# Optimization experiments

Hardware: AMD Instinct MI355X
Metric: run time of the kernel (lower is better)

## Reference

```python
import jax, jax.numpy as jnp
import numpy as np

N_EMBD = 384
N_HEAD = 6
HEAD_SIZE = N_EMBD // N_HEAD  # 64
BLOCK = 64
EPS = 1e-5


def _layernorm(x, g, b):
    mu = jnp.mean(x, axis=-1, keepdims=True)
    var = jnp.mean(jnp.square(x - mu), axis=-1, keepdims=True)
    return (x - mu) * jax.lax.rsqrt(var + EPS) * g + b


def setup_inputs() -> dict:
    key = jax.random.key(0)
    ks = jax.random.split(key, 12)
    s = 0.02
    return {
        "x": jax.random.normal(ks[0], (1024, BLOCK, N_EMBD), dtype=jnp.float32),
        "ln1_g": jnp.ones((N_EMBD,), jnp.float32),
        "ln1_b": jnp.zeros((N_EMBD,), jnp.float32),
        "Wq": jax.random.normal(ks[1], (N_HEAD, N_EMBD, HEAD_SIZE), jnp.float32) * s,
        "Wk": jax.random.normal(ks[2], (N_HEAD, N_EMBD, HEAD_SIZE), jnp.float32) * s,
        "Wv": jax.random.normal(ks[3], (N_HEAD, N_EMBD, HEAD_SIZE), jnp.float32) * s,
        "Wo": jax.random.normal(ks[4], (N_EMBD, N_EMBD), jnp.float32) * s,
        "bo": jnp.zeros((N_EMBD,), jnp.float32),
        "ln2_g": jnp.ones((N_EMBD,), jnp.float32),
        "ln2_b": jnp.zeros((N_EMBD,), jnp.float32),
        "W1": jax.random.normal(ks[5], (N_EMBD, 4 * N_EMBD), jnp.float32) * s,
        "b1": jnp.zeros((4 * N_EMBD,), jnp.float32),
        "W2": jax.random.normal(ks[6], (4 * N_EMBD, N_EMBD), jnp.float32) * s,
        "b2": jnp.zeros((N_EMBD,), jnp.float32),
    }


def reference(x, ln1_g, ln1_b, Wq, Wk, Wv, Wo, bo, ln2_g, ln2_b, W1, b1, W2, b2):
    B, T, C = x.shape
    # --- multi-head causal self-attention on ln1(x) ---
    xn = _layernorm(x, ln1_g, ln1_b)
    q = jnp.einsum('btc,hcd->bhtd', xn, Wq)
    k = jnp.einsum('btc,hcd->bhtd', xn, Wk)
    v = jnp.einsum('btc,hcd->bhtd', xn, Wv)
    scale = HEAD_SIZE ** -0.5
    att = jnp.einsum('bhtd,bhsd->bhts', q, k) * scale
    causal = jnp.tril(jnp.ones((T, T), bool))
    att = jnp.where(causal, att, -jnp.inf)
    att = jax.nn.softmax(att, axis=-1)  # dropout is identity at eval
    out = jnp.einsum('bhts,bhsd->bhtd', att, v)
    out = out.transpose(0, 2, 1, 3).reshape(B, T, C)  # concat heads
    x = x + out @ Wo + bo
    # --- feed-forward on ln2(x) ---
    xn2 = _layernorm(x, ln2_g, ln2_b)
    h = jax.nn.relu(xn2 @ W1 + b1)
    x = x + h @ W2 + b2
    return x
```

## Files before the change

kernel.cpp:

```cpp
#include <hip/hip_runtime.h>

#define TT 64
#define CC 384
#define NH 6
#define HID 1536
#define LDX 392
#define LDH 72

typedef __bf16 bf16x8 __attribute__((ext_vector_type(8)));
typedef float f32x4 __attribute__((ext_vector_type(4)));
typedef unsigned short us8 __attribute__((ext_vector_type(8)));

#define MFMA(a, b, c) __builtin_amdgcn_mfma_f32_16x16x32_bf16(a, b, c, 0, 0, 0)
#define WAITVM(N) asm volatile("s_waitcnt vmcnt(" #N ")" ::: "memory")

static __device__ __forceinline__ unsigned short f2bf(float f) {
  unsigned u = __builtin_bit_cast(unsigned, f);
  u += 0x7FFFu + ((u >> 16) & 1u);
  return (unsigned short)(u >> 16);
}
static __device__ __forceinline__ float bf2f(unsigned short h) {
  unsigned u = ((unsigned)h) << 16;
  return __builtin_bit_cast(float, u);
}
static __device__ __forceinline__ bf16x8 ld8(const unsigned short* p) {
  return __builtin_bit_cast(bf16x8, *reinterpret_cast<const us8*>(p));
}
static __device__ __forceinline__ void glds16(const unsigned short* g, unsigned short* l) {
  __builtin_amdgcn_global_load_lds(
      (const __attribute__((address_space(1))) void*)g,
      (__attribute__((address_space(3))) void*)l, 16, 0, 0);
}

__global__ void prep_w(const float* __restrict__ Wq, const float* __restrict__ Wk,
                       const float* __restrict__ Wv, const float* __restrict__ Wo,
                       const float* __restrict__ W1, const float* __restrict__ W2,
                       unsigned short* __restrict__ ws) {
  const int T0 = 1152 * 384;
  const int T1 = T0 + 384 * 384;
  const int T2 = T1 + 1536 * 384;
  const int T3 = T2 + 384 * 1536;
  for (int i = blockIdx.x * blockDim.x + threadIdx.x; i < T3; i += gridDim.x * blockDim.x) {
    float v;
    if (i < T0) {
      int n = i / 384, k = i % 384;
      int hh = n / 192, j = n % 192;
      const float* W = (j < 64) ? Wq : (j < 128) ? Wk : Wv;
      int d = (j < 64) ? j : (j < 128) ? j - 64 : j - 128;
      v = W[((size_t)hh * 384 + k) * 64 + d];
    } else if (i < T1) {
      int i2 = i - T0; int n = i2 / 384, k = i2 % 384;
      v = Wo[(size_t)k * 384 + n];
    } else if (i < T2) {
      int i2 = i - T1; int n = i2 / 384, k = i2 % 384;
      v = W1[(size_t)k * 1536 + n];
    } else {
      int i2 = i - T2; int n = i2 / 1536, k = i2 % 1536;
      v = W2[(size_t)k * 384 + n];
    }
    ws[i] = f2bf(v);
  }
}

__global__ __launch_bounds__(256, 2)
void attn_fwd(const float* __restrict__ x,
              const float* __restrict__ ln1g, const float* __restrict__ ln1b,
              const float* __restrict__ bo,
              const unsigned short* __restrict__ Wqkv,
              const unsigned short* __restrict__ WoT,
              float* __restrict__ x2) {
  __shared__ unsigned short sXN[TT * LDX];
  __shared__ unsigned short sHEAD[3 * TT * LDH];
  unsigned short* sQ = sHEAD;
  unsigned short* sK = sHEAD + TT * LDH;
  unsigned short* sV = sHEAD + 2 * TT * LDH;

  const int b = blockIdx.x;
  const int tid = threadIdx.x;
  const int wv = tid >> 6;
  const int ln = tid & 63;
  const int l16 = ln & 15;
  const int lg = ln >> 4;
  const float* xb = x + (size_t)b * TT * CC;
  const f32x4 Z4 = {0.f, 0.f, 0.f, 0.f};

#pragma unroll 1
  for (int r = wv * 16; r < wv * 16 + 16; ++r) {
    float v[6], s = 0.f, sq = 0.f;
#pragma unroll
    for (int j = 0; j < 6; ++j) { v[j] = xb[r * CC + ln + 64 * j]; s += v[j]; sq += v[j] * v[j]; }
#pragma unroll
    for (int off = 32; off; off >>= 1) { s += __shfl_xor(s, off); sq += __shfl_xor(sq, off); }
    float mu = s * (1.f / CC);
    float rs = rsqrtf(sq * (1.f / CC) - mu * mu + 1e-5f);
#pragma unroll
    for (int j = 0; j < 6; ++j) {
      int c = ln + 64 * j;
      sXN[r * LDX + c] = f2bf((v[j] - mu) * rs * ln1g[c] + ln1b[c]);
    }
  }
  __syncthreads();

  f32x4 pacc[4][6];
#pragma unroll
  for (int m = 0; m < 4; ++m)
#pragma unroll
    for (int c = 0; c < 6; ++c) pacc[m][c] = Z4;

  const unsigned short* prow[6];
#pragma unroll
  for (int c = 0; c < 6; ++c)
    prow[c] = WoT + (size_t)(wv * 96 + c * 16 + l16) * CC + 8 * lg;

#pragma unroll 1
  for (int h = 0; h < NH; ++h) {
    const unsigned short* wrow[3];
#pragma unroll
    for (int c = 0; c < 3; ++c)
      wrow[c] = Wqkv + (size_t)(h * 192 + wv * 48 + c * 16 + l16) * CC + 8 * lg;

    f32x4 qacc[4][3];
#pragma unroll
    for (int m = 0; m < 4; ++m)
#pragma unroll
      for (int c = 0; c < 3; ++c) qacc[m][c] = Z4;

    bf16x8 bpre[2][3];
#pragma unroll
    for (int c = 0; c < 3; ++c) bpre[0][c] = ld8(wrow[c] + 0);
#pragma unroll
    for (int c = 0; c < 3; ++c) bpre[1][c] = ld8(wrow[c] + 32);
#pragma unroll
    for (int kk = 0; kk < CC; kk += 32) {
      const int slot = (kk >> 5) & 1;
      bf16x8 bcur[3];
#pragma unroll
      for (int c = 0; c < 3; ++c) bcur[c] = bpre[slot][c];
      if (kk + 64 < CC) {
#pragma unroll
        for (int c = 0; c < 3; ++c) bpre[slot][c] = ld8(wrow[c] + kk + 64);
      }
      bf16x8 a[4];
#pragma unroll
      for (int m = 0; m < 4; ++m)
        a[m] = ld8(&sXN[(m * 16 + l16) * LDX + kk + 8 * lg]);
      __builtin_amdgcn_s_setprio(1);
#pragma unroll
      for (int c = 0; c < 3; ++c)
#pragma unroll
        for (int m = 0; m < 4; ++m) qacc[m][c] = MFMA(a[m], bcur[c], qacc[m][c]);
      __builtin_amdgcn_s_setprio(0);
    }
    __syncthreads();
#pragma unroll
    for (int m = 0; m < 4; ++m)
#pragma unroll
      for (int c = 0; c < 3; ++c) {
        int n = wv * 48 + c * 16 + l16;
#pragma unroll
        for (int rg = 0; rg < 4; ++rg) {
          int t = m * 16 + lg * 4 + rg;
          unsigned short bv = f2bf(qacc[m][c][rg]);
          if (n < 64) sQ[t * LDH + n] = bv;
          else if (n < 128) sK[t * LDH + (n - 64)] = bv;
          else sV[(n - 128) * LDH + t] = bv;
        }
      }
    __syncthreads();

    f32x4 sacc[4];
#pragma unroll
    for (int c = 0; c < 4; ++c) sacc[c] = Z4;
#pragma unroll
    for (int kk = 0; kk < 64; kk += 32) {
      bf16x8 a = ld8(&sQ[(wv * 16 + l16) * LDH + kk + 8 * lg]);
#pragma unroll
      for (int c = 0; c < 4; ++c) {
        bf16x8 bb = ld8(&sK[(c * 16 + l16) * LDH + kk + 8 * lg]);
        sacc[c] = MFMA(a, bb, sacc[c]);
      }
    }
#pragma unroll
    for (int rg = 0; rg < 4; ++rg) {
      int row = wv * 16 + lg * 4 + rg;
      float e[4], mx = -1e30f;
#pragma unroll
      for (int c = 0; c < 4; ++c) {
        int col = c * 16 + l16;
        float vv = sacc[c][rg] * 0.125f;
        e[c] = (col <= row) ? vv : -1e30f;
        mx = fmaxf(mx, e[c]);
      }
#pragma unroll
      for (int off = 8; off; off >>= 1) mx = fmaxf(mx, __shfl_xor(mx, off));
      float sum = 0.f;
#pragma unroll
      for (int c = 0; c < 4; ++c) {
        int col = c * 16 + l16;
        e[c] = (col <= row) ? __expf(e[c] - mx) : 0.f;
        sum += e[c];
      }
#pragma unroll
      for (int off = 8; off; off >>= 1) sum += __shfl_xor(sum, off);
      float inv = 1.f / sum;
#pragma unroll
      for (int c = 0; c < 4; ++c)
        sQ[row * LDH + c * 16 + l16] = f2bf(e[c] * inv);
    }

    bf16x8 pb[2][6];
#pragma unroll
    for (int s2 = 0; s2 < 2; ++s2)
#pragma unroll
      for (int c = 0; c < 6; ++c)
        pb[s2][c] = ld8(prow[c] + h * 64 + 32 * s2);

    f32x4 oacc[4];
#pragma unroll
    for (int c = 0; c < 4; ++c) oacc[c] = Z4;
#pragma unroll
    for (int kk = 0; kk < 64; kk += 32) {
      bf16x8 a = ld8(&sQ[(wv * 16 + l16) * LDH + kk + 8 * lg]);
#pragma unroll
      for (int c = 0; c < 4; ++c) {
        bf16x8 bb = ld8(&sV[(c * 16 + l16) * LDH + kk + 8 * lg]);
        oacc[c] = MFMA(a, bb, oacc[c]);
      }
    }
    __syncthreads();
#pragma unroll
    for (int c = 0; c < 4; ++c)
#pragma unroll
      for (int rg = 0; rg < 4; ++rg) {
        int t = wv * 16 + lg * 4 + rg;
        sK[t * LDH + c * 16 + l16] = f2bf(oacc[c][rg]);
      }
    __syncthreads();

    __builtin_amdgcn_s_setprio(1);
#pragma unroll
    for (int kk = 0; kk < 64; kk += 32) {
      const int slot = kk >> 5;
      bf16x8 a[4];
#pragma unroll
      for (int m = 0; m < 4; ++m)
        a[m] = ld8(&sK[(m * 16 + l16) * LDH + kk + 8 * lg]);
#pragma unroll
      for (int c = 0; c < 6; ++c)
#pragma unroll
        for (int m = 0; m < 4; ++m) pacc[m][c] = MFMA(a[m], pb[slot][c], pacc[m][c]);
    }
    __builtin_amdgcn_s_setprio(0);
  }

  float* xo = x2 + (size_t)b * TT * CC;
#pragma unroll
  for (int m = 0; m < 4; ++m)
#pragma unroll
    for (int c = 0; c < 6; ++c) {
      int n = wv * 96 + c * 16 + l16;
      float bov = bo[n];
#pragma unroll
      for (int rg = 0; rg < 4; ++rg) {
        int t = m * 16 + lg * 4 + rg;
        xo[t * CC + n] = xb[t * CC + n] + pacc[m][c][rg] + bov;
      }
    }
}

__global__ __launch_bounds__(256, 2)
void mlp_fwd(const float* __restrict__ ln2g, const float* __restrict__ ln2b,
             const float* __restrict__ b1, const float* __restrict__ b2,
             const unsigned short* __restrict__ W1T,
             const unsigned short* __restrict__ W2T,
             float* xo) {
  __shared__ unsigned short sXN[24576];
  __shared__ unsigned short sH[8192];
  __shared__ unsigned short sW[8192];

  const int b = blockIdx.x;
  const int tid = threadIdx.x;
  const int wv = tid >> 6;
  const int ln = tid & 63;
  const int l16 = ln & 15;
  const int lg = ln >> 4;
  float* xb = xo + (size_t)b * TT * CC;
  const f32x4 Z4 = {0.f, 0.f, 0.f, 0.f};
  unsigned short* myW = sW + wv * 2048;
  const int rx = (l16 ^ lg) << 3;

#pragma unroll 1
  for (int r = wv * 16; r < wv * 16 + 16; ++r) {
    float v[6], s = 0.f, sq = 0.f;
#pragma unroll
    for (int j = 0; j < 6; ++j) { v[j] = xb[r * CC + ln + 64 * j]; s += v[j]; sq += v[j] * v[j]; }
#pragma unroll
    for (int off = 32; off; off >>= 1) { s += __shfl_xor(s, off); sq += __shfl_xor(sq, off); }
    float mu = s * (1.f / CC);
    float rs = rsqrtf(sq * (1.f / CC) - mu * mu + 1e-5f);
    int m = r >> 4, row16 = r & 15;
#pragma unroll
    for (int j = 0; j < 6; ++j) {
      int c = ln + 64 * j;
      int sl = c >> 5, ks = (c >> 3) & 3, off = c & 7;
      sXN[(((m * 12 + sl) * 4 + ks) * 16 + (row16 ^ ks)) * 8 + off] =
          f2bf((v[j] - mu) * rs * ln2g[c] + ln2b[c]);
    }
  }
  __syncthreads();

#define G1S(CH, SL) do {                                                        \
    _Pragma("unroll")                                                           \
    for (int j = 0; j < 2; ++j)                                                 \
      glds16(W1T + (size_t)((CH) * 128 + wv * 32 + j * 16 + (ln >> 2)) * CC +   \
                 (SL) * 32 + (ln & 3) * 8,                                      \
             myW + ((SL) & 1) * 1024 + j * 512);                                \
  } while (0)

#define G1C(SL) do {                                                            \
    bf16x8 a_[4];                                                               \
    _Pragma("unroll")                                                           \
    for (int m = 0; m < 4; ++m)                                                 \
      a_[m] = ld8(&sXN[((m * 48 + (SL) * 4 + lg) << 7) + rx]);                  \
    __builtin_amdgcn_s_setprio(1);                                              \
    _Pragma("unroll")                                                           \
    for (int c = 0; c < 2; ++c) {                                               \
      bf16x8 bb_ = ld8(&myW[((SL) & 1) * 1024 + c * 512 + l16 * 32 + lg * 8]);  \
      _Pragma("unroll")                                                         \
      for (int m = 0; m < 4; ++m) hacc[m][c] = MFMA(a_[m], bb_, hacc[m][c]);    \
    }                                                                           \
    __builtin_amdgcn_s_setprio(0);                                              \
  } while (0)

  f32x4 macc[4][6];
#pragma unroll
  for (int m = 0; m < 4; ++m)
#pragma unroll
    for (int c = 0; c < 6; ++c) macc[m][c] = Z4;

  const unsigned short* w2base = W2T + (size_t)(wv * 96 + l16) * HID + 8 * lg;

  G1S(0, 0);

#pragma unroll 1
  for (int ch = 0; ch < 12; ++ch) {
    f32x4 hacc[4][2];
#pragma unroll
    for (int m = 0; m < 4; ++m)
#pragma unroll
      for (int c = 0; c < 2; ++c) hacc[m][c] = Z4;

    G1S(ch, 1);  WAITVM(2); G1C(0);
    G1S(ch, 2);  WAITVM(2); G1C(1);
    G1S(ch, 3);  WAITVM(2); G1C(2);
    G1S(ch, 4);  WAITVM(2); G1C(3);
    G1S(ch, 5);  WAITVM(2); G1C(4);
    G1S(ch, 6);  WAITVM(2); G1C(5);
    G1S(ch, 7);  WAITVM(2); G1C(6);
    G1S(ch, 8);  WAITVM(2); G1C(7);
    G1S(ch, 9);  WAITVM(2); G1C(8);
    G1S(ch, 10); WAITVM(2); G1C(9);
    G1S(ch, 11); WAITVM(2); G1C(10);
    WAITVM(0);   G1C(11);

    float b1c[2];
#pragma unroll
    for (int c = 0; c < 2; ++c) b1c[c] = b1[ch * 128 + wv * 32 + c * 16 + l16];
    const unsigned short* w2p = w2base + ch * 128;
    bf16x8 c2[6];
#pragma unroll
    for (int c = 0; c < 6; ++c) c2[c] = ld8(w2p + (size_t)(c * 16) * HID);
    if (ch < 11) G1S(ch + 1, 0);

    __syncthreads();

#pragma unroll
    for (int m = 0; m < 4; ++m)
#pragma unroll
      for (int c = 0; c < 2; ++c) {
        int nl = wv * 32 + c * 16 + l16;
        int slh = nl >> 5, ks = (nl >> 3) & 3, off = nl & 7;
#pragma unroll
        for (int rg = 0; rg < 4; ++rg) {
          int row16 = lg * 4 + rg;
          sH[(((m * 4 + slh) * 4 + ks) * 16 + (row16 ^ ks)) * 8 + off] =
              f2bf(fmaxf(hacc[m][c][rg] + b1c[c], 0.f));
        }
      }
    __syncthreads();

#pragma unroll
    for (int sl = 0; sl < 4; ++sl) {
      bf16x8 a2[4];
#pragma unroll
      for (int m = 0; m < 4; ++m)
        a2[m] = ld8(&sH[((m * 16 + sl * 4 + lg) << 7) + rx]);
      bf16x8 nxt[6];
      if (sl < 3) {
#pragma unroll
        for (int c = 0; c < 6; ++c) nxt[c] = ld8(w2p + (size_t)(c * 16) * HID + (sl + 1) * 32);
      }
      __builtin_amdgcn_s_setprio(1);
#pragma unroll
      for (int c = 0; c < 6; ++c)
#pragma unroll
        for (int m = 0; m < 4; ++m) macc[m][c] = MFMA(a2[m], c2[c], macc[m][c]);
      __builtin_amdgcn_s_setprio(0);
      if (sl < 3) {
#pragma unroll
        for (int c = 0; c < 6; ++c) c2[c] = nxt[c];
      }
    }
  }

#pragma unroll
  for (int m = 0; m < 4; ++m)
#pragma unroll
    for (int c = 0; c < 6; ++c) {
      int n = wv * 96 + c * 16 + l16;
      float b2v = b2[n];
#pragma unroll
      for (int rg = 0; rg < 4; ++rg) {
        int t = m * 16 + lg * 4 + rg;
        size_t idx = (size_t)t * CC + n;
        float x2v = xb[idx];
        xb[idx] = x2v + macc[m][c][rg] + b2v;
      }
    }
#undef G1S
#undef G1C
}

extern "C" void kernel_launch(void* const* d_in, const int* in_sizes, int n_in,
                              void* d_out, int out_size, void* d_ws, size_t ws_size,
                              hipStream_t stream) {
  const float* x    = (const float*)d_in[0];
  const float* ln1g = (const float*)d_in[1];
  const float* ln1b = (const float*)d_in[2];
  const float* Wq   = (const float*)d_in[3];
  const float* Wk   = (const float*)d_in[4];
  const float* Wv   = (const float*)d_in[5];
  const float* Wo   = (const float*)d_in[6];
  const float* bo   = (const float*)d_in[7];
  const float* ln2g = (const float*)d_in[8];
  const float* ln2b = (const float*)d_in[9];
  const float* W1   = (const float*)d_in[10];
  const float* b1   = (const float*)d_in[11];
  const float* W2   = (const float*)d_in[12];
  const float* b2   = (const float*)d_in[13];
  unsigned short* ws = (unsigned short*)d_ws;

  const size_t need = (size_t)(1152 * 384 + 384 * 384 + 1536 * 384 + 384 * 1536) * 2;
  if (ws_size < need) return;

  hipLaunchKernelGGL(prep_w, dim3(1024), dim3(256), 0, stream, Wq, Wk, Wv, Wo, W1, W2, ws);

  const unsigned short* Wqkv = ws;
  const unsigned short* WoT  = ws + 1152 * 384;
  const unsigned short* W1T  = WoT + 384 * 384;
  const unsigned short* W2T  = W1T + 1536 * 384;
  int nblk = in_sizes[0] / (TT * CC);

  hipLaunchKernelGGL(attn_fwd, dim3(nblk), dim3(256), 0, stream,
                     x, ln1g, ln1b, bo, Wqkv, WoT, (float*)d_out);
  hipLaunchKernelGGL(mlp_fwd, dim3(nblk), dim3(256), 0, stream,
                     ln2g, ln2b, b1, b2, W1T, W2T, (float*)d_out);
}
```

Before: 440.8 us.

## Fuse attention and MLP kernels into a single per-batch block kernel

Merges the attention and MLP kernels into one kernel that keeps the post-attention residual in registers. LayerNorm2 statistics are computed through a small cross-wave shared-memory reduction instead of re-reading x2 from global memory. This removes one kernel launch and the global round trip of the intermediate activations. Shared memory is aliased into an 80KB buffer, which may limit occupancy to two blocks per CU and lengthens each block's critical path.

```diff
diff --git a/kernel.cpp b/kernel.cpp
--- a/kernel.cpp
+++ b/kernel.cpp
@@ -63,17 +63,26 @@
 }
 
 __global__ __launch_bounds__(256, 2)
-void attn_fwd(const float* __restrict__ x,
-              const float* __restrict__ ln1g, const float* __restrict__ ln1b,
-              const float* __restrict__ bo,
-              const unsigned short* __restrict__ Wqkv,
-              const unsigned short* __restrict__ WoT,
-              float* __restrict__ x2) {
-  __shared__ unsigned short sXN[TT * LDX];
-  __shared__ unsigned short sHEAD[3 * TT * LDH];
-  unsigned short* sQ = sHEAD;
-  unsigned short* sK = sHEAD + TT * LDH;
-  unsigned short* sV = sHEAD + 2 * TT * LDH;
+void block_fused(const float* __restrict__ x,
+                 const float* __restrict__ ln1g, const float* __restrict__ ln1b,
+                 const float* __restrict__ bo,
+                 const float* __restrict__ ln2g, const float* __restrict__ ln2b,
+                 const float* __restrict__ b1, const float* __restrict__ b2,
+                 const unsigned short* __restrict__ Wqkv,
+                 const unsigned short* __restrict__ WoT,
+                 const unsigned short* __restrict__ W1T,
+                 const unsigned short* __restrict__ W2T,
+                 float* __restrict__ out) {
+  __shared__ __align__(16) unsigned char smem[81920];
+  unsigned short* sXN1 = (unsigned short*)smem;
+  unsigned short* sQ = (unsigned short*)(smem + 50176);
+  unsigned short* sK = sQ + TT * LDH;
+  unsigned short* sV = sK + TT * LDH;
+  float2* stats = (float2*)(smem + 77824);
+  float2* murs  = (float2*)(smem + 79872);
+  unsigned short* sXN2 = (unsigned short*)smem;
+  unsigned short* sH   = (unsigned short*)(smem + 49152);
+  unsigned short* sWl  = (unsigned short*)(smem + 65536);
 
   const int b = blockIdx.x;
   const int tid = threadIdx.x;
@@ -82,7 +91,10 @@
   const int l16 = ln & 15;
   const int lg = ln >> 4;
   const float* xb = x + (size_t)b * TT * CC;
+  float* xo = out + (size_t)b * TT * CC;
   const f32x4 Z4 = {0.f, 0.f, 0.f, 0.f};
+  unsigned short* myW = sWl + wv * 2048;
+  const int rx = (l16 ^ lg) << 3;
 
 #pragma unroll 1
   for (int r = wv * 16; r < wv * 16 + 16; ++r) {
@@ -96,7 +108,7 @@
 #pragma unroll
     for (int j = 0; j < 6; ++j) {
       int c = ln + 64 * j;
-      sXN[r * LDX + c] = f2bf((v[j] - mu) * rs * ln1g[c] + ln1b[c]);
+      sXN1[r * LDX + c] = f2bf((v[j] - mu) * rs * ln1g[c] + ln1b[c]);
     }
   }
   __syncthreads();
@@ -143,7 +155,7 @@
       bf16x8 a[4];
 #pragma unroll
       for (int m = 0; m < 4; ++m)
-        a[m] = ld8(&sXN[(m * 16 + l16) * LDX + kk + 8 * lg]);
+        a[m] = ld8(&sXN1[(m * 16 + l16) * LDX + kk + 8 * lg]);
       __builtin_amdgcn_s_setprio(1);
 #pragma unroll
       for (int c = 0; c < 3; ++c)
@@ -253,7 +265,6 @@
     __builtin_amdgcn_s_setprio(0);
   }
 
-  float* xo = x2 + (size_t)b * TT * CC;
 #pragma unroll
   for (int m = 0; m < 4; ++m)
 #pragma unroll
@@ -263,51 +274,53 @@
 #pragma unroll
       for (int rg = 0; rg < 4; ++rg) {
         int t = m * 16 + lg * 4 + rg;
-        xo[t * CC + n] = xb[t * CC + n] + pacc[m][c][rg] + bov;
-      }
-    }
-}
-
-__global__ __launch_bounds__(256, 2)
-void mlp_fwd(const float* __restrict__ ln2g, const float* __restrict__ ln2b,
-             const float* __restrict__ b1, const float* __restrict__ b2,
-             const unsigned short* __restrict__ W1T,
-             const unsigned short* __restrict__ W2T,
-             float* xo) {
-  __shared__ unsigned short sXN[24576];
-  __shared__ unsigned short sH[8192];
-  __shared__ unsigned short sW[8192];
-
-  const int b = blockIdx.x;
-  const int tid = threadIdx.x;
-  const int wv = tid >> 6;
-  const int ln = tid & 63;
-  const int l16 = ln & 15;
-  const int lg = ln >> 4;
-  float* xb = xo + (size_t)b * TT * CC;
-  const f32x4 Z4 = {0.f, 0.f, 0.f, 0.f};
-  unsigned short* myW = sW + wv * 2048;
-  const int rx = (l16 ^ lg) << 3;
-
-#pragma unroll 1
-  for (int r = wv * 16; r < wv * 16 + 16; ++r) {
-    float v[6], s = 0.f, sq = 0.f;
-#pragma unroll
-    for (int j = 0; j < 6; ++j) { v[j] = xb[r * CC + ln + 64 * j]; s += v[j]; sq += v[j] * v[j]; }
-#pragma unroll
-    for (int off = 32; off; off >>= 1) { s += __shfl_xor(s, off); sq += __shfl_xor(sq, off); }
+        float v = xb[t * CC + n] + pacc[m][c][rg] + bov;
+        pacc[m][c][rg] = v;
+        xo[t * CC + n] = v;
+      }
+    }
+#pragma unroll
+  for (int m = 0; m < 4; ++m)
+#pragma unroll
+    for (int rg = 0; rg < 4; ++rg) {
+      float s = 0.f, sq = 0.f;
+#pragma unroll
+      for (int c = 0; c < 6; ++c) { float v = pacc[m][c][rg]; s += v; sq += v * v; }
+#pragma unroll
+      for (int off = 1; off < 16; off <<= 1) { s += __shfl_xor(s, off); sq += __shfl_xor(sq, off); }
+      if (l16 == 0) {
+        float2 p; p.x = s; p.y = sq;
+        stats[(m * 16 + lg * 4 + rg) * 4 + wv] = p;
+      }
+    }
+  __syncthreads();
+  if (ln < 16) {
+    int t = wv * 16 + ln;
+    float s = 0.f, sq = 0.f;
+#pragma unroll
+    for (int w2 = 0; w2 < 4; ++w2) { float2 p = stats[t * 4 + w2]; s += p.x; sq += p.y; }
     float mu = s * (1.f / CC);
-    float rs = rsqrtf(sq * (1.f / CC) - mu * mu + 1e-5f);
-    int m = r >> 4, row16 = r & 15;
-#pragma unroll
-    for (int j = 0; j < 6; ++j) {
-      int c = ln + 64 * j;
-      int sl = c >> 5, ks = (c >> 3) & 3, off = c & 7;
-      sXN[(((m * 12 + sl) * 4 + ks) * 16 + (row16 ^ ks)) * 8 + off] =
-          f2bf((v[j] - mu) * rs * ln2g[c] + ln2b[c]);
-    }
+    float2 mr; mr.x = mu; mr.y = rsqrtf(sq * (1.f / CC) - mu * mu + 1e-5f);
+    murs[t] = mr;
   }
   __syncthreads();
+#pragma unroll
+  for (int m = 0; m < 4; ++m)
+#pragma unroll
+    for (int rg = 0; rg < 4; ++rg) {
+      int t = m * 16 + lg * 4 + rg;
+      float2 mr = murs[t];
+      int row16 = lg * 4 + rg;
+#pragma unroll
+      for (int c = 0; c < 6; ++c) {
+        int n = wv * 96 + c * 16 + l16;
+        int sl = n >> 5, ks = (n >> 3) & 3, off = n & 7;
+        sXN2[(((m * 12 + sl) * 4 + ks) * 16 + (row16 ^ ks)) * 8 + off] =
+            f2bf((pacc[m][c][rg] - mr.x) * mr.y * ln2g[n] + ln2b[n]);
+      }
+    }
+  __syncthreads();
+  WAITVM(0);
 
 #define G1S(CH, SL) do {                                                        \
     _Pragma("unroll")                                                           \
@@ -316,12 +329,11 @@
                  (SL) * 32 + (ln & 3) * 8,                                      \
              myW + ((SL) & 1) * 1024 + j * 512);                                \
   } while (0)
-
 #define G1C(SL) do {                                                            \
     bf16x8 a_[4];                                                               \
     _Pragma("unroll")                                                           \
     for (int m = 0; m < 4; ++m)                                                 \
-      a_[m] = ld8(&sXN[((m * 48 + (SL) * 4 + lg) << 7) + rx]);                  \
+      a_[m] = ld8(&sXN2[((m * 48 + (SL) * 4 + lg) << 7) + rx]);                 \
     __builtin_amdgcn_s_setprio(1);                                              \
     _Pragma("unroll")                                                           \
     for (int c = 0; c < 2; ++c) {                                               \
@@ -341,7 +353,6 @@
   const unsigned short* w2base = W2T + (size_t)(wv * 96 + l16) * HID + 8 * lg;
 
   G1S(0, 0);
-
 #pragma unroll 1
   for (int ch = 0; ch < 12; ++ch) {
     f32x4 hacc[4][2];
@@ -423,8 +434,8 @@
       for (int rg = 0; rg < 4; ++rg) {
         int t = m * 16 + lg * 4 + rg;
         size_t idx = (size_t)t * CC + n;
-        float x2v = xb[idx];
-        xb[idx] = x2v + macc[m][c][rg] + b2v;
+        float x2v = xo[idx];
+        xo[idx] = x2v + macc[m][c][rg] + b2v;
       }
     }
 #undef G1S
@@ -461,8 +472,7 @@
   const unsigned short* W2T  = W1T + 1536 * 384;
   int nblk = in_sizes[0] / (TT * CC);
 
-  hipLaunchKernelGGL(attn_fwd, dim3(nblk), dim3(256), 0, stream,
-                     x, ln1g, ln1b, bo, Wqkv, WoT, (float*)d_out);
-  hipLaunchKernelGGL(mlp_fwd, dim3(nblk), dim3(256), 0, stream,
-                     ln2g, ln2b, b1, b2, W1T, W2T, (float*)d_out);
-}
+  hipLaunchKernelGGL(block_fused, dim3(nblk), dim3(256), 0, stream,
+                     x, ln1g, ln1b, bo, ln2g, ln2b, b1, b2,
+                     Wqkv, WoT, W1T, W2T, (float*)d_out);
+}
```

Result: slower. 515.9 us (+17.0%).
